# Optimization experiments

Hardware: AMD Instinct MI355X
Metric: run time of the kernel (lower is better)

The kernel has to match this reference:

```python
import jax, jax.numpy as jnp
import numpy as np

B = 1024       # batch of graphs
NUM = 512      # predicates / nodes per graph
D = 64         # embedding_dim
H = 64         # hidden_dim
E = 4096       # edges per graph (shared structure across batch)
MAIN_NUM = 10  # softmax segment [0, MAIN_NUM); sigmoid on the rest


def setup_inputs() -> dict:
    key = jax.random.key(0)
    ks = jax.random.split(key, 8)
    x = jax.random.uniform(ks[0], (B, NUM), dtype=jnp.float32)
    embedding = jax.random.normal(ks[1], (NUM, D), dtype=jnp.float32) * 0.1
    W1 = jax.random.normal(ks[2], (D, H), dtype=jnp.float32) * (1.0 / np.sqrt(D))
    b1 = jnp.zeros((H,), jnp.float32)
    W2 = jax.random.normal(ks[3], (H, H), dtype=jnp.float32) * (1.0 / np.sqrt(H))
    b2 = jnp.zeros((H,), jnp.float32)
    W3 = jax.random.normal(ks[4], (H, 1), dtype=jnp.float32) * (1.0 / np.sqrt(H))
    b3 = jnp.zeros((1,), jnp.float32)
    edge_row = jax.random.randint(ks[5], (E,), 0, NUM, dtype=jnp.int32)
    edge_col = jax.random.randint(ks[6], (E,), 0, NUM, dtype=jnp.int32)
    return {"x": x, "embedding": embedding, "W1": W1, "b1": b1,
            "W2": W2, "b2": b2, "W3": W3, "b3": b3,
            "edge_row": edge_row, "edge_col": edge_col}


def _gcn_layer(h, W, b, row, col, norm):
    # h: [B, NUM, in]; GCNConv = linear -> D^{-1/2} A D^{-1/2} aggregate -> +bias
    hW = jnp.einsum('bni,io->bno', h, W)                 # [B, NUM, out]
    msg = hW[:, row, :] * norm[None, :, None]            # [B, E, out]
    agg = jnp.zeros_like(hW).at[:, col, :].add(msg)      # scatter to targets
    return agg + b


def reference(x, embedding, W1, b1, W2, b2, W3, b3, edge_row, edge_col):
    num = x.shape[1]
    # symmetric GCN normalization (add_self_loops=False, unit edge weights)
    deg = jnp.zeros((num,), x.dtype).at[edge_col].add(1.0)
    dinv = jnp.where(deg > 0, jax.lax.rsqrt(jnp.maximum(deg, 1.0)), 0.0)
    norm = dinv[edge_row] * dinv[edge_col]               # [E]

    h = x[..., None] * embedding                         # [B, NUM, D]
    h = jax.nn.relu(_gcn_layer(h, W1, b1, edge_row, edge_col, norm))
    h = jax.nn.relu(_gcn_layer(h, W2, b2, edge_row, edge_col, norm))
    logits = _gcn_layer(h, W3, b3, edge_row, edge_col, norm)[..., 0]  # [B, NUM]

    # convert_to_confidence: softmax over multiclass segment, sigmoid elsewhere
    phi_sm = jax.nn.softmax(logits[:, :MAIN_NUM], axis=1)
    phi_sg = jax.nn.sigmoid(logits[:, MAIN_NUM:])
    return jnp.concatenate([phi_sm, phi_sg], axis=1)
```

## Files before the change

### kernel.cpp

```cpp
#include <hip/hip_runtime.h>
#include <stdint.h>

#define NB    1024
#define NUM   512
#define HD    64
#define NE    4096
#define NEP   4608
#define MAIN  10
#define HBS   72

typedef _Float16 hlf;
typedef __attribute__((ext_vector_type(2))) _Float16 hlf2;
typedef __attribute__((ext_vector_type(8))) _Float16 hlf8;
typedef __attribute__((ext_vector_type(4))) float f32x4;

__device__ __forceinline__ unsigned short f2h(float f) {
    hlf v = (hlf)f;
    return __builtin_bit_cast(unsigned short, v);
}

__global__ __launch_bounds__(512) void prep_all(
    const int* __restrict__ erow, const int* __restrict__ ecol,
    const float* __restrict__ emb, const float* __restrict__ W1,
    const float* __restrict__ W2,
    int* __restrict__ rsptr, int* __restrict__ colmap, int* __restrict__ epk,
    short* __restrict__ E1, short* __restrict__ W2T)
{
    const int t = threadIdx.x;
    if (blockIdx.x != 0) {
        int g = (blockIdx.x - 1) * 512 + t;
        if (g < NUM * HD) {
            int node = g >> 6, dim = g & 63;
            float acc = 0.0f;
            #pragma unroll
            for (int k = 0; k < HD; ++k) acc += emb[node * HD + k] * W1[k * HD + dim];
            E1[g] = (short)f2h(acc);
        } else if (g < NUM * HD + HD * HD) {
            int j = g - NUM * HD;
            int dout = j >> 6, din = j & 63;
            W2T[j] = (short)f2h(W2[din * HD + dout]);
        }
        return;
    }

    __shared__ int   sdeg[NUM];
    __shared__ int   aux[NUM];
    __shared__ float sdv[NUM];
    __shared__ int   rnk[NUM];
    __shared__ int   rdg[NUM];
    __shared__ int   wsum[8];

    const int lane = t & 63, wv = t >> 6;

    sdeg[t] = 0; aux[t] = 0;
    __syncthreads();
    for (int e = t; e < NE; e += 512) atomicAdd(&sdeg[ecol[e]], 1);
    __syncthreads();
    const int deg  = sdeg[t];
    const int pdeg = (deg + 1) & ~1;
    const int dbin = deg < NUM ? deg : NUM - 1;
    sdv[t] = deg > 0 ? rsqrtf((float)deg) : 0.0f;
    atomicAdd(&aux[dbin], 1);
    __syncthreads();
    {
        int v = aux[t];
        #pragma unroll
        for (int ofs = 1; ofs < 64; ofs <<= 1) {
            int sh = __shfl_up(v, ofs, 64);
            if (lane >= ofs) v += sh;
        }
        if (lane == 63) wsum[wv] = v;
        __syncthreads();
        if (t == 0) {
            int s = 0;
            #pragma unroll
            for (int w = 0; w < 8; ++w) { int tmp = wsum[w]; wsum[w] = s; s += tmp; }
        }
        __syncthreads();
        int inc = v + wsum[wv];
        aux[t]  = inc;
        __syncthreads();
        sdeg[t] = (t == 0) ? 0 : aux[t - 1];
        __syncthreads();
    }
    {
        int r = atomicAdd(&sdeg[dbin], 1);
        rnk[t] = r;
        rdg[r] = pdeg;
        colmap[r] = t;
    }
    __syncthreads();
    {
        int dv = rdg[t], v = dv;
        #pragma unroll
        for (int ofs = 1; ofs < 64; ofs <<= 1) {
            int sh = __shfl_up(v, ofs, 64);
            if (lane >= ofs) v += sh;
        }
        if (lane == 63) wsum[wv] = v;
        __syncthreads();
        if (t == 0) {
            int s = 0;
            #pragma unroll
            for (int w = 0; w < 8; ++w) { int tmp = wsum[w]; wsum[w] = s; s += tmp; }
        }
        __syncthreads();
        int inc  = v + dv ? (v + wsum[wv]) : (v + wsum[wv]);
        inc = v + wsum[wv];
        int excl = inc - dv;
        rsptr[t] = excl;
        if (t == NUM - 1) rsptr[NUM] = inc;
        aux[t] = excl;
        __syncthreads();
    }
    sdeg[t] = aux[rnk[t]];
    __syncthreads();
    for (int i = t; i < NEP; i += 512) epk[i] = 0;
    __syncthreads();
    for (int e = t; e < NE; e += 512) {
        int c = ecol[e], rr = erow[e];
        int p = atomicAdd(&sdeg[c], 1);
        unsigned ns = (unsigned)f2h(sdv[rr] * sdv[c]);
        epk[p] = (rr << 23) | (int)ns;
    }
}

__global__ __launch_bounds__(1024, 4) void gcn_body(
    const float* __restrict__ x, const hlf* __restrict__ E1,
    const hlf* __restrict__ W2T,
    const float* __restrict__ b1, const float* __restrict__ b2,
    const float* __restrict__ W3, const float* __restrict__ b3,
    const int* __restrict__ rsptrg, const int* __restrict__ colmap,
    const int* __restrict__ epkg,
    float* __restrict__ out)
{
    __shared__ hlf HA[NUM * HD];
    __shared__ hlf HB[NUM * HBS];
    __shared__ int eps[NEP];
    __shared__ int sptr[513];
    __shared__ float sred[2];

    float* tv   = (float*)HB;
    float* slog = ((float*)HB) + NUM;

    const int t     = threadIdx.x;
    const int b     = blockIdx.x;
    const int lane  = t & 63;
    const int wave  = t >> 6;
    const int q     = lane >> 4;
    const int l15   = lane & 15;
    const int grp   = lane >> 3;
    const int dbase = (lane & 7) * 8;

    {
        const int4* g4 = (const int4*)epkg;
        *(int4*)&eps[t * 4] = g4[t];
        if (t < 128) *(int4*)&eps[4096 + t * 4] = g4[1024 + t];
    }
    if (t < 513) sptr[t] = rsptrg[t];

    #pragma unroll
    for (int p = 0; p < 4; ++p) {
        int i = t + p * 1024;
        int r = i >> 3, d8 = (i & 7) * 8;
        float xr = x[b * NUM + r];
        hlf  xh = (hlf)xr;
        hlf8 e  = *(const hlf8*)&E1[r * HD + d8];
        hlf8 o;
        #pragma unroll
        for (int j = 0; j < 8; ++j) o[j] = e[j] * xh;
        *(hlf8*)&HA[r * HD + d8] = o;
    }

    float b1v[8], b2v[8], w3v[8];
    {
        f32x4 u0 = *(const f32x4*)&b1[dbase], u1 = *(const f32x4*)&b1[dbase + 4];
        f32x4 v0 = *(const f32x4*)&b2[dbase], v1 = *(const f32x4*)&b2[dbase + 4];
        f32x4 w0 = *(const f32x4*)&W3[dbase], w1 = *(const f32x4*)&W3[dbase + 4];
        #pragma unroll
        for (int j = 0; j < 4; ++j) {
            b1v[j] = u0[j]; b1v[j + 4] = u1[j];
            b2v[j] = v0[j]; b2v[j + 4] = v1[j];
            w3v[j] = w0[j]; w3v[j + 4] = w1[j];
        }
    }
    const char* HAb = (const char*)HA + dbase * 2;
    __syncthreads();

#define LDROW(d, pe) d = *(const uint4*)(HAb + ((unsigned)(pe) >> 16));
#define MACROW(hv, pe) {                                                      \
        const hlf nh = __builtin_bit_cast(hlf2, (unsigned)(pe))[0];           \
        const hlf2 p0 = __builtin_bit_cast(hlf2, (hv).x);                     \
        const hlf2 p1 = __builtin_bit_cast(hlf2, (hv).y);                     \
        const hlf2 p2 = __builtin_bit_cast(hlf2, (hv).z);                     \
        const hlf2 p3 = __builtin_bit_cast(hlf2, (hv).w);                     \
        a[0] = fmaf((float)p0[0], (float)nh, a[0]);                           \
        a[1] = fmaf((float)p0[1], (float)nh, a[1]);                           \
        a[2] = fmaf((float)p1[0], (float)nh, a[2]);                           \
        a[3] = fmaf((float)p1[1], (float)nh, a[3]);                           \
        a[4] = fmaf((float)p2[0], (float)nh, a[4]);                           \
        a[5] = fmaf((float)p2[1], (float)nh, a[5]);                           \
        a[6] = fmaf((float)p3[0], (float)nh, a[6]);                           \
        a[7] = fmaf((float)p3[1], (float)nh, a[7]); }

#define CHUNK8 {                                                              \
        int2 qa = *(const int2*)&eps[e];     int2 qb = *(const int2*)&eps[e + 2]; \
        int2 qc = *(const int2*)&eps[e + 4]; int2 qd = *(const int2*)&eps[e + 6]; \
        uint4 v0, v1, v2, v3, v4, v5, v6, v7;                                 \
        LDROW(v0, qa.x) LDROW(v1, qa.y) LDROW(v2, qb.x) LDROW(v3, qb.y)       \
        LDROW(v4, qc.x) LDROW(v5, qc.y) LDROW(v6, qd.x) LDROW(v7, qd.y)       \
        MACROW(v0, qa.x) MACROW(v1, qa.y) MACROW(v2, qb.x) MACROW(v3, qb.y)   \
        MACROW(v4, qc.x) MACROW(v5, qc.y) MACROW(v6, qd.x) MACROW(v7, qd.y) }
#define CHUNK4 {                                                              \
        int2 qa = *(const int2*)&eps[e];     int2 qb = *(const int2*)&eps[e + 2]; \
        uint4 v0, v1, v2, v3;                                                 \
        LDROW(v0, qa.x) LDROW(v1, qa.y) LDROW(v2, qb.x) LDROW(v3, qb.y)       \
        MACROW(v0, qa.x) MACROW(v1, qa.y) MACROW(v2, qb.x) MACROW(v3, qb.y) }
#define CHUNK2 {                                                              \
        int2 qa = *(const int2*)&eps[e];                                      \
        uint4 v0, v1;                                                         \
        LDROW(v0, qa.x) LDROW(v1, qa.y)                                       \
        MACROW(v0, qa.x) MACROW(v1, qa.y) }

    #pragma unroll 1
    for (int set = 0; set < 4; ++set) {
        int r  = set * 128 + wave * 8 + grp;
        int e0 = sptr[r], e1 = sptr[r + 1];
        int c  = colmap[r];
        float a[8];
        #pragma unroll
        for (int j = 0; j < 8; ++j) a[j] = 0.0f;
        int e = e0;
        for (; e + 8 <= e1; e += 8) CHUNK8;
        if (e + 4 <= e1) { CHUNK4; e += 4; }
        if (e < e1) CHUNK2;
        uint4 ov;
        ov.x = __builtin_bit_cast(unsigned, __builtin_amdgcn_cvt_pkrtz(
                   fmaxf(a[0] + b1v[0], 0.0f), fmaxf(a[1] + b1v[1], 0.0f)));
        ov.y = __builtin_bit_cast(unsigned, __builtin_amdgcn_cvt_pkrtz(
                   fmaxf(a[2] + b1v[2], 0.0f), fmaxf(a[3] + b1v[3], 0.0f)));
        ov.z = __builtin_bit_cast(unsigned, __builtin_amdgcn_cvt_pkrtz(
                   fmaxf(a[4] + b1v[4], 0.0f), fmaxf(a[5] + b1v[5], 0.0f)));
        ov.w = __builtin_bit_cast(unsigned, __builtin_amdgcn_cvt_pkrtz(
                   fmaxf(a[6] + b1v[6], 0.0f), fmaxf(a[7] + b1v[7], 0.0f)));
        *(uint4*)&HB[c * HBS + dbase] = ov;
    }
    __syncthreads();

    {
        hlf8 bfr[2][4];
        #pragma unroll
        for (int ks = 0; ks < 2; ++ks)
            #pragma unroll
            for (int nt = 0; nt < 4; ++nt)
                bfr[ks][nt] = *(const hlf8*)&W2T[(nt * 16 + l15) * HD + ks * 32 + q * 8];
        f32x4 acc[2][4];
        #pragma unroll
        for (int mt = 0; mt < 2; ++mt)
            #pragma unroll
            for (int nt = 0; nt < 4; ++nt) acc[mt][nt] = (f32x4){0.f, 0.f, 0.f, 0.f};
        const int mbase = wave * 32;
        #pragma unroll
        for (int mt = 0; mt < 2; ++mt)
            #pragma unroll
            for (int ks = 0; ks < 2; ++ks) {
                hlf8 af = *(const hlf8*)&HB[(mbase + mt * 16 + l15) * HBS
                                            + ks * 32 + q * 8];
                #pragma unroll
                for (int nt = 0; nt < 4; ++nt)
                    acc[mt][nt] = __builtin_amdgcn_mfma_f32_16x16x32_f16(
                        af, bfr[ks][nt], acc[mt][nt], 0, 0, 0);
            }
        #pragma unroll
        for (int mt = 0; mt < 2; ++mt)
            #pragma unroll
            for (int nt = 0; nt < 4; ++nt)
                #pragma unroll
                for (int i = 0; i < 4; ++i)
                    HA[(mbase + mt * 16 + q * 4 + i) * HD + nt * 16 + l15] =
                        (hlf)acc[mt][nt][i];
    }
    __syncthreads();

    #pragma unroll 1
    for (int set = 0; set < 4; ++set) {
        int r  = set * 128 + wave * 8 + grp;
        int e0 = sptr[r], e1 = sptr[r + 1];
        int c  = colmap[r];
        float a[8];
        #pragma unroll
        for (int j = 0; j < 8; ++j) a[j] = 0.0f;
        int e = e0;
        for (; e + 8 <= e1; e += 8) CHUNK8;
        if (e + 4 <= e1) { CHUNK4; e += 4; }
        if (e < e1) CHUNK2;
        float v = 0.0f;
        #pragma unroll
        for (int j = 0; j < 8; ++j)
            v += fmaxf(a[j] + b2v[j], 0.0f) * w3v[j];
        v += __shfl_xor(v, 1, 64);
        v += __shfl_xor(v, 2, 64);
        v += __shfl_xor(v, 4, 64);
        if ((lane & 7) == 0) tv[c] = v;
    }
    __syncthreads();

    {
        int rk = t >> 1, hh = t & 1;
        int e0 = sptr[rk], e1 = sptr[rk + 1];
        int mid = (e0 + e1) >> 1;
        int ea = hh ? mid : e0;
        int eb = hh ? e1 : mid;
        float acc = 0.0f;
        for (int e = ea; e < eb; ++e) {
            unsigned pe = (unsigned)eps[e];
            float nf = (float)__builtin_bit_cast(hlf2, pe)[0];
            acc = fmaf(nf, *(const float*)((const char*)tv + (pe >> 21)), acc);
        }
        acc += __shfl_xor(acc, 1, 64);
        if (!hh) slog[colmap[rk]] = acc + b3[0];
    }
    __syncthreads();

    if (t < 64) {
        float v = (t < MAIN) ? slog[t] : -1e30f;
        float m = v;
        m = fmaxf(m, __shfl_xor(m, 1, 64));
        m = fmaxf(m, __shfl_xor(m, 2, 64));
        m = fmaxf(m, __shfl_xor(m, 4, 64));
        m = fmaxf(m, __shfl_xor(m, 8, 64));
        float ev = (t < MAIN) ? __expf(v - m) : 0.0f;
        ev += __shfl_xor(ev, 1, 64);
        ev += __shfl_xor(ev, 2, 64);
        ev += __shfl_xor(ev, 4, 64);
        ev += __shfl_xor(ev, 8, 64);
        if (t == 0) { sred[0] = m; sred[1] = ev; }
    }
    __syncthreads();

    if (t < NUM) {
        float l = slog[t];
        float o = (t < MAIN) ? __expf(l - sred[0]) / sred[1]
                             : 1.0f / (1.0f + __expf(-l));
        out[b * NUM + t] = o;
    }
#undef LDROW
#undef MACROW
#undef CHUNK8
#undef CHUNK4
#undef CHUNK2
}

extern "C" void kernel_launch(void* const* d_in, const int* in_sizes, int n_in,
                              void* d_out, int out_size, void* d_ws, size_t ws_size,
                              hipStream_t stream) {
    const float* x    = (const float*)d_in[0];
    const float* emb  = (const float*)d_in[1];
    const float* W1   = (const float*)d_in[2];
    const float* b1   = (const float*)d_in[3];
    const float* W2   = (const float*)d_in[4];
    const float* b2   = (const float*)d_in[5];
    const float* W3   = (const float*)d_in[6];
    const float* b3   = (const float*)d_in[7];
    const int*   erow = (const int*)d_in[8];
    const int*   ecol = (const int*)d_in[9];

    char* ws = (char*)d_ws;
    int*   rsptr  = (int*)ws;
    int*   colmap = (int*)(ws + 2176);
    int*   epk    = (int*)(ws + 4224);
    short* E1     = (short*)(ws + 22656);
    short* W2T    = (short*)(ws + 88192);

    prep_all<<<73, 512, 0, stream>>>(erow, ecol, emb, W1, W2,
                                     rsptr, colmap, epk, E1, W2T);
    gcn_body<<<NB, 1024, 0, stream>>>(x, (const hlf*)E1, (const hlf*)W2T,
                                      b1, b2, W3, b3,
                                      rsptr, colmap, epk, (float*)d_out);
}
```

Measured before the change: 155.4 us.

## Software-pipeline SpMM gather loop and alternate wave row assignment for balance

```diff
diff --git a/kernel.cpp b/kernel.cpp
--- a/kernel.cpp
+++ b/kernel.cpp
@@ -105,8 +105,7 @@
             for (int w = 0; w < 8; ++w) { int tmp = wsum[w]; wsum[w] = s; s += tmp; }
         }
         __syncthreads();
-        int inc  = v + dv ? (v + wsum[wv]) : (v + wsum[wv]);
-        inc = v + wsum[wv];
+        int inc  = v + wsum[wv];
         int excl = inc - dv;
         rsptr[t] = excl;
         if (t == NUM - 1) rsptr[NUM] = inc;
@@ -136,7 +135,7 @@
 {
     __shared__ hlf HA[NUM * HD];
     __shared__ hlf HB[NUM * HBS];
-    __shared__ int eps[NEP];
+    __shared__ int eps[NEP + 8];
     __shared__ int sptr[513];
     __shared__ float sred[2];
 
@@ -156,6 +155,7 @@
         const int4* g4 = (const int4*)epkg;
         *(int4*)&eps[t * 4] = g4[t];
         if (t < 128) *(int4*)&eps[4096 + t * 4] = g4[1024 + t];
+        if (t < 8)   eps[NEP + t] = 0;
     }
     if (t < 513) sptr[t] = rsptrg[t];
 
@@ -203,37 +203,33 @@
         a[6] = fmaf((float)p3[0], (float)nh, a[6]);                           \
         a[7] = fmaf((float)p3[1], (float)nh, a[7]); }
 
-#define CHUNK8 {                                                              \
-        int2 qa = *(const int2*)&eps[e];     int2 qb = *(const int2*)&eps[e + 2]; \
-        int2 qc = *(const int2*)&eps[e + 4]; int2 qd = *(const int2*)&eps[e + 6]; \
-        uint4 v0, v1, v2, v3, v4, v5, v6, v7;                                 \
-        LDROW(v0, qa.x) LDROW(v1, qa.y) LDROW(v2, qb.x) LDROW(v3, qb.y)       \
-        LDROW(v4, qc.x) LDROW(v5, qc.y) LDROW(v6, qd.x) LDROW(v7, qd.y)       \
-        MACROW(v0, qa.x) MACROW(v1, qa.y) MACROW(v2, qb.x) MACROW(v3, qb.y)   \
-        MACROW(v4, qc.x) MACROW(v5, qc.y) MACROW(v6, qd.x) MACROW(v7, qd.y) }
-#define CHUNK4 {                                                              \
-        int2 qa = *(const int2*)&eps[e];     int2 qb = *(const int2*)&eps[e + 2]; \
-        uint4 v0, v1, v2, v3;                                                 \
-        LDROW(v0, qa.x) LDROW(v1, qa.y) LDROW(v2, qb.x) LDROW(v3, qb.y)       \
-        MACROW(v0, qa.x) MACROW(v1, qa.y) MACROW(v2, qb.x) MACROW(v3, qb.y) }
-#define CHUNK2 {                                                              \
-        int2 qa = *(const int2*)&eps[e];                                      \
-        uint4 v0, v1;                                                         \
-        LDROW(v0, qa.x) LDROW(v1, qa.y)                                       \
-        MACROW(v0, qa.x) MACROW(v1, qa.y) }
+#define SPMM_PIPE(E0, E1v)                                                    \
+    int e = E0;                                                               \
+    int2 qa0 = *(const int2*)&eps[e], qb0 = *(const int2*)&eps[e + 2];        \
+    uint4 u0, u1, u2, u3;                                                     \
+    LDROW(u0, qa0.x) LDROW(u1, qa0.y) LDROW(u2, qb0.x) LDROW(u3, qb0.y)       \
+    for (; e + 4 < E1v; e += 4) {                                             \
+        int2 qa1 = *(const int2*)&eps[e + 4];                                 \
+        int2 qb1 = *(const int2*)&eps[e + 6];                                 \
+        uint4 w0, w1, w2, w3;                                                 \
+        LDROW(w0, qa1.x) LDROW(w1, qa1.y) LDROW(w2, qb1.x) LDROW(w3, qb1.y)   \
+        MACROW(u0, qa0.x) MACROW(u1, qa0.y)                                   \
+        MACROW(u2, qb0.x) MACROW(u3, qb0.y)                                   \
+        qa0 = qa1; qb0 = qb1; u0 = w0; u1 = w1; u2 = w2; u3 = w3;             \
+    }                                                                         \
+    if (e < E1v)     { MACROW(u0, qa0.x) MACROW(u1, qa0.y) }                  \
+    if (e + 2 < E1v) { MACROW(u2, qb0.x) MACROW(u3, qb0.y) }
 
     #pragma unroll 1
     for (int set = 0; set < 4; ++set) {
-        int r  = set * 128 + wave * 8 + grp;
+        int wv8 = ((set & 1) ? (15 - wave) : wave) * 8;
+        int r  = set * 128 + wv8 + grp;
         int e0 = sptr[r], e1 = sptr[r + 1];
         int c  = colmap[r];
         float a[8];
         #pragma unroll
         for (int j = 0; j < 8; ++j) a[j] = 0.0f;
-        int e = e0;
-        for (; e + 8 <= e1; e += 8) CHUNK8;
-        if (e + 4 <= e1) { CHUNK4; e += 4; }
-        if (e < e1) CHUNK2;
+        { SPMM_PIPE(e0, e1) }
         uint4 ov;
         ov.x = __builtin_bit_cast(unsigned, __builtin_amdgcn_cvt_pkrtz(
                    fmaxf(a[0] + b1v[0], 0.0f), fmaxf(a[1] + b1v[1], 0.0f)));
@@ -284,16 +280,14 @@
 
     #pragma unroll 1
     for (int set = 0; set < 4; ++set) {
-        int r  = set * 128 + wave * 8 + grp;
+        int wv8 = ((set & 1) ? (15 - wave) : wave) * 8;
+        int r  = set * 128 + wv8 + grp;
         int e0 = sptr[r], e1 = sptr[r + 1];
         int c  = colmap[r];
         float a[8];
         #pragma unroll
         for (int j = 0; j < 8; ++j) a[j] = 0.0f;
-        int e = e0;
-        for (; e + 8 <= e1; e += 8) CHUNK8;
-        if (e + 4 <= e1) { CHUNK4; e += 4; }
-        if (e < e1) CHUNK2;
+        { SPMM_PIPE(e0, e1) }
         float v = 0.0f;
         #pragma unroll
         for (int j = 0; j < 8; ++j)
@@ -346,9 +340,7 @@
     }
 #undef LDROW
 #undef MACROW
-#undef CHUNK8
-#undef CHUNK4
-#undef CHUNK2
+#undef SPMM_PIPE
 }
 
 extern "C" void kernel_launch(void* const* d_in, const int* in_sizes, int n_in,
```

Result: slower. 158.5 us (+2.0%).
